# Kernel tuning notes

Hardware: AMD Instinct MI355X
Metric: run time of the kernel (lower is better)

The kernel has to match this reference:

```python
import jax, jax.numpy as jnp
import numpy as np

N_USERS = 100000
M_ITEMS = 50000
N = N_USERS + M_ITEMS
D = 64
NNZ = 4800000
N_LAYERS = 3


def spmm(idx, val, x):
    # sparse COO (idx[0]=rows, idx[1]=cols) @ dense x : gather-scale-scatter
    rows, cols = idx[0], idx[1]
    return jax.ops.segment_sum(val[:, None] * x[cols], rows, num_segments=N)


def propagate(idx, val, emb0):
    # LightGCN propagation: mean over layer-0..n_layers embeddings
    embs = [emb0]
    e = emb0
    for _ in range(N_LAYERS):
        e = spmm(idx, val, e)
        embs.append(e)
    return jnp.mean(jnp.stack(embs, axis=1), axis=1)  # [N, D]


def setup_inputs() -> dict:
    key = jax.random.key(0)
    ks = jax.random.split(key, 10)
    return {
        "emb_im": 0.1 * jax.random.normal(ks[0], (N, D), jnp.float32),
        "emb_q": 0.1 * jax.random.normal(ks[1], (N, D), jnp.float32),
        "emb_p": 0.1 * jax.random.normal(ks[2], (N, D), jnp.float32),
        "g_im_idx": jax.random.randint(ks[3], (2, NNZ), 0, N, jnp.int32),
        "g_im_val": jax.random.uniform(ks[4], (NNZ,), jnp.float32) / 32.0,
        "g_q_idx": jax.random.randint(ks[5], (2, NNZ), 0, N, jnp.int32),
        "g_q_val": jax.random.uniform(ks[6], (NNZ,), jnp.float32) / 32.0,
        "g_p_idx": jax.random.randint(ks[7], (2, NNZ), 0, N, jnp.int32),
        "g_p_val": jax.random.uniform(ks[8], (NNZ,), jnp.float32) / 32.0,
        "add_weight": jnp.ones((3,), jnp.float32),
    }


def reference(emb_im, emb_q, emb_p, g_im_idx, g_im_val, g_q_idx, g_q_val,
              g_p_idx, g_p_val, add_weight):
    out_im = propagate(g_im_idx, g_im_val, emb_im)
    out_q = propagate(g_q_idx, g_q_val, emb_q)
    out_p = propagate(g_p_idx, g_p_val, emb_p)
    # weighted_add over factors: sum_f w_f * out_f ; users/items split is a
    # row split of this combined [N, D] matrix
    stacked = jnp.stack([out_im, out_q, out_p], axis=0)  # [3, N, D]
    combined = jnp.sum(stacked * add_weight[:, None, None], axis=0)  # [N, D]
    return combined  # rows [:N_USERS] = users, rows [N_USERS:] = items
```

## Files before the change

### kernel.cpp

```cpp
#include <hip/hip_runtime.h>

#define N_TOTAL 150000
#define DIM 64
#define RPB 293
#define NBUCK 512
#define MAGIC 14658592u
#define CAP 10368
#define CHUNK 8192

typedef float v2f __attribute__((ext_vector_type(2)));

__global__ void fill_bcur_kernel(int* __restrict__ bcur) {
    int t = blockIdx.x * 256 + threadIdx.x;
    if (t < NBUCK) bcur[t] = t * CAP;
}

__global__ void bin_kernel(const int* __restrict__ idx, const float* __restrict__ val,
                           int* __restrict__ bcur, unsigned* __restrict__ bcs,
                           unsigned short* __restrict__ brl, int nnz) {
    __shared__ unsigned scs[CHUNK];
    __shared__ unsigned srow[CHUNK];
    __shared__ int lcnt[NBUCK];
    __shared__ int lstart[NBUCK];
    __shared__ int gbase[NBUCK];
    __shared__ int wsum[8];
    int t = threadIdx.x;
    int base = blockIdx.x * CHUNK;
    int nEdges = min(CHUNK, nnz - base);
    lcnt[t] = 0;
    __syncthreads();
    unsigned mycs[16];
    int myrow[16], myb[16];
    #pragma unroll
    for (int i = 0; i < 16; ++i) {
        int e = base + t + i * 512;
        if (e < nnz) {
            int r = idx[e];
            int b = (int)__umulhi((unsigned)r, MAGIC);
            myb[i] = b;
            myrow[i] = r;
            unsigned vbits = (__float_as_uint(val[e]) + 0x20000u) & 0xFFFC0000u;
            mycs[i] = vbits | (unsigned)idx[nnz + e];
            atomicAdd(&lcnt[b], 1);
        } else {
            myb[i] = -1;
        }
    }
    __syncthreads();
    int c = lcnt[t];
    int lane = t & 63, wid = t >> 6;
    int incl = c;
    #pragma unroll
    for (int d = 1; d < 64; d <<= 1) {
        int y = __shfl_up(incl, d, 64);
        if (lane >= d) incl += y;
    }
    if (lane == 63) wsum[wid] = incl;
    __syncthreads();
    if (t == 0) {
        int s0 = 0;
        #pragma unroll
        for (int i = 0; i < 8; ++i) { int tmp = wsum[i]; wsum[i] = s0; s0 += tmp; }
    }
    __syncthreads();
    int excl = incl - c + wsum[wid];
    lstart[t] = excl;
    gbase[t] = c ? atomicAdd(&bcur[t], c) : 0;
    lcnt[t] = 0;
    __syncthreads();
    #pragma unroll
    for (int i = 0; i < 16; ++i) {
        int b = myb[i];
        if (b >= 0) {
            int o = atomicAdd(&lcnt[b], 1);
            int p = lstart[b] + o;
            scs[p] = mycs[i];
            srow[p] = (unsigned)myrow[i];
        }
    }
    __syncthreads();
    for (int p = t; p < nEdges; p += 512) {
        int r = (int)srow[p];
        int b = (int)__umulhi((unsigned)r, MAGIC);
        int dst = gbase[b] + (p - lstart[b]);
        if (dst < (b + 1) * CAP) {
            bcs[dst] = scs[p];
            brl[dst] = (unsigned short)(r - b * RPB);
        }
    }
}


__device__ void scatterc_body(int b, const unsigned* __restrict__ bcs,
                              const unsigned short* __restrict__ brl,
                              int* __restrict__ bcur,
                              int* __restrict__ rlo, int* __restrict__ rhi,
                              unsigned* __restrict__ cs2) {
    __shared__ int hist[RPB];
    __shared__ int ssc[256];
    int t = threadIdx.x;
    int s = b * CAP, e = min(bcur[b], s + CAP);
    for (int i = t; i < RPB; i += 256) hist[i] = 0;
    __syncthreads();
    for (int k = s + t; k < e; k += 256)
        atomicAdd(&hist[brl[k]], 1);
    __syncthreads();
    int i0 = 2 * t;
    int c0 = (i0 < RPB) ? hist[i0] : 0;
    int c1 = (i0 + 1 < RPB) ? hist[i0 + 1] : 0;
    int s2 = c0 + c1;
    ssc[t] = s2;
    __syncthreads();
    for (int off = 1; off < 256; off <<= 1) {
        int x = (t >= off) ? ssc[t - off] : 0;
        __syncthreads();
        ssc[t] += x;
        __syncthreads();
    }
    int excl = ssc[t] - s2;
    __syncthreads();
    int base0 = s + excl, base1 = s + excl + c0;
    if (i0 < RPB) {
        int row = b * RPB + i0;
        if (row < N_TOTAL) { rlo[row] = base0; rhi[row] = base0 + c0; }
        hist[i0] = base0;
    }
    if (i0 + 1 < RPB) {
        int row = b * RPB + i0 + 1;
        if (row < N_TOTAL) { rlo[row] = base1; rhi[row] = base1 + c1; }
        hist[i0 + 1] = base1;
    }
    __syncthreads();
    for (int k = s + t; k < e; k += 256) {
        int rl_ = brl[k];
        int o = atomicAdd(&hist[rl_], 1);
        cs2[o] = bcs[k];
    }
    __syncthreads();
    if (t == 0) bcur[b] = s;
}

__device__ void conv_body(int i, const float* __restrict__ x, unsigned* __restrict__ y,
                          int nwords) {
    if (i >= nwords) return;
    int row = i >> 4, w_ = i & 15;
    const float* xr = x + ((size_t)row << 6) + w_;
    int p = __builtin_amdgcn_cvt_pk_fp8_f32(xr[0] * 64.f, xr[16] * 64.f, 0, false);
    p = __builtin_amdgcn_cvt_pk_fp8_f32(xr[32] * 64.f, xr[48] * 64.f, p, true);
    y[i] = (unsigned)p;
}

__device__ inline float4 dec_sum3(const unsigned* __restrict__ T, int i, int nwords) {
    unsigned a = T[i], b = T[i + nwords], c = T[i + 2 * nwords];
    v2f alo = __builtin_amdgcn_cvt_pk_f32_fp8((int)a, false);
    v2f ahi = __builtin_amdgcn_cvt_pk_f32_fp8((int)a, true);
    v2f blo = __builtin_amdgcn_cvt_pk_f32_fp8((int)b, false);
    v2f bhi = __builtin_amdgcn_cvt_pk_f32_fp8((int)b, true);
    v2f clo = __builtin_amdgcn_cvt_pk_f32_fp8((int)c, false);
    v2f chi = __builtin_amdgcn_cvt_pk_f32_fp8((int)c, true);
    float4 r;
    r.x = alo.x + blo.x + clo.x;
    r.y = alo.y + blo.y + clo.y;
    r.z = ahi.x + bhi.x + chi.x;
    r.w = ahi.y + bhi.y + chi.y;
    return r;
}

__device__ void combine_body(int i, const float* __restrict__ emb,
                             const unsigned* __restrict__ T, float c,
                             float* __restrict__ out, int nwords, bool first) {
    if (i >= nwords) return;
    const float kInv = 1.f / 64.f;
    int r = i >> 4, wd = i & 15;
    size_t base = ((size_t)r << 6) + wd;
    float4 s = dec_sum3(T, i, nwords);
    float v0 = c * (emb[base] + kInv * s.x);
    float v1 = c * (emb[base + 16] + kInv * s.y);
    float v2 = c * (emb[base + 32] + kInv * s.z);
    float v3 = c * (emb[base + 48] + kInv * s.w);
    if (first) {
        out[base] = v0; out[base + 16] = v1; out[base + 32] = v2; out[base + 48] = v3;
    } else {
        out[base] += v0; out[base + 16] += v1; out[base + 32] += v2; out[base + 48] += v3;
    }
}

__global__ void scv_kernel(const unsigned* __restrict__ bcs,
                           const unsigned short* __restrict__ brl,
                           int* __restrict__ bcur, int* __restrict__ rlo,
                           int* __restrict__ rhi, unsigned* __restrict__ cs2,
                           const float* __restrict__ embf, unsigned* __restrict__ emb8,
                           const float* __restrict__ embp, const unsigned* __restrict__ Tp,
                           const float* __restrict__ w, int fprev, float* __restrict__ out,
                           int nwords, int nCvt) {
    int b = blockIdx.x;
    if (b < NBUCK) {
        scatterc_body(b, bcs, brl, bcur, rlo, rhi, cs2);
        return;
    }
    b -= NBUCK;
    if (b < nCvt) {
        conv_body(b * 256 + (int)threadIdx.x, embf, emb8, nwords);
        return;
    }
    b -= nCvt;
    combine_body(b * 256 + (int)threadIdx.x, embp, Tp, w[fprev] * 0.25f, out, nwords,
                 fprev == 0);
}

__global__ void combine_kernel(const float* __restrict__ emb, const unsigned* __restrict__ T,
                               const float* __restrict__ w, int f, float* __restrict__ out,
                               int nwords) {
    combine_body(blockIdx.x * 256 + (int)threadIdx.x, emb, T, w[f] * 0.25f, out, nwords,
                 false);
}

__global__ void combine3_kernel(const float* __restrict__ e0, const float* __restrict__ e1,
                                const float* __restrict__ e2, const unsigned* __restrict__ t0,
                                const unsigned* __restrict__ t1, const unsigned* __restrict__ t2,
                                const float* __restrict__ w, float* __restrict__ out,
                                int nwords) {
    int i = blockIdx.x * blockDim.x + threadIdx.x;
    if (i >= nwords) return;
    const float kInv = 1.f / 64.f;
    float c0 = w[0] * 0.25f, c1 = w[1] * 0.25f, c2 = w[2] * 0.25f;
    int r = i >> 4, wd = i & 15;
    size_t base = ((size_t)r << 6) + wd;
    float4 s0 = dec_sum3(t0, i, nwords);
    float4 s1 = dec_sum3(t1, i, nwords);
    float4 s2 = dec_sum3(t2, i, nwords);
    out[base]      = c0 * (e0[base]      + kInv * s0.x) + c1 * (e1[base]      + kInv * s1.x)
                   + c2 * (e2[base]      + kInv * s2.x);
    out[base + 16] = c0 * (e0[base + 16] + kInv * s0.y) + c1 * (e1[base + 16] + kInv * s1.y)
                   + c2 * (e2[base + 16] + kInv * s2.y);
    out[base + 32] = c0 * (e0[base + 32] + kInv * s0.z) + c1 * (e1[base + 32] + kInv * s1.z)
                   + c2 * (e2[base + 32] + kInv * s2.z);
    out[base + 48] = c0 * (e0[base + 48] + kInv * s0.w) + c1 * (e1[base + 48] + kInv * s1.w)
                   + c2 * (e2[base + 48] + kInv * s2.w);
}

__global__ void spmm_reg_kernel(const int* __restrict__ rlo, const int* __restrict__ rhi,
                                const unsigned* __restrict__ cs, const uint2* __restrict__ x2,
                                uint2* __restrict__ y2, int nrows) {
    int gid = blockIdx.x * blockDim.x + threadIdx.x;
    int row = gid >> 6;
    int lane = gid & 63;
    if (row >= nrows) return;
    int s = rlo[row], e = rhi[row];
    int q = lane >> 3, sub = lane & 7;
    v2f a0 = {0.f, 0.f}, a1 = {0.f, 0.f}, a2 = {0.f, 0.f}, a3 = {0.f, 0.f};
    v2f b0 = {0.f, 0.f}, b1 = {0.f, 0.f}, b2 = {0.f, 0.f}, b3 = {0.f, 0.f};
    int k = s + q;
    for (; k + 8 < e; k += 16) {
        unsigned ed0 = cs[k], ed1 = cs[k + 8];
        uint2 g0 = x2[((size_t)(ed0 & 0x3FFFFu) << 3) + sub];
        uint2 g1 = x2[((size_t)(ed1 & 0x3FFFFu) << 3) + sub];
        float v0 = __uint_as_float(ed0 & 0xFFFC0000u);
        float v1 = __uint_as_float(ed1 & 0xFFFC0000u);
        v2f vv0 = {v0, v0}, vv1 = {v1, v1};
        a0 += vv0 * __builtin_amdgcn_cvt_pk_f32_fp8((int)g0.x, false);
        a1 += vv0 * __builtin_amdgcn_cvt_pk_f32_fp8((int)g0.x, true);
        a2 += vv0 * __builtin_amdgcn_cvt_pk_f32_fp8((int)g0.y, false);
        a3 += vv0 * __builtin_amdgcn_cvt_pk_f32_fp8((int)g0.y, true);
        b0 += vv1 * __builtin_amdgcn_cvt_pk_f32_fp8((int)g1.x, false);
        b1 += vv1 * __builtin_amdgcn_cvt_pk_f32_fp8((int)g1.x, true);
        b2 += vv1 * __builtin_amdgcn_cvt_pk_f32_fp8((int)g1.y, false);
        b3 += vv1 * __builtin_amdgcn_cvt_pk_f32_fp8((int)g1.y, true);
    }
    for (; k < e; k += 8) {
        unsigned ed = cs[k];
        uint2 g = x2[((size_t)(ed & 0x3FFFFu) << 3) + sub];
        float vv = __uint_as_float(ed & 0xFFFC0000u);
        v2f vv2 = {vv, vv};
        a0 += vv2 * __builtin_amdgcn_cvt_pk_f32_fp8((int)g.x, false);
        a1 += vv2 * __builtin_amdgcn_cvt_pk_f32_fp8((int)g.x, true);
        a2 += vv2 * __builtin_amdgcn_cvt_pk_f32_fp8((int)g.y, false);
        a3 += vv2 * __builtin_amdgcn_cvt_pk_f32_fp8((int)g.y, true);
    }
    a0 += b0; a1 += b1; a2 += b2; a3 += b3;
    float r0 = a0.x, r1 = a0.y, r2 = a1.x, r3 = a1.y;
    float r4 = a2.x, r5 = a2.y, r6 = a3.x, r7 = a3.y;
    r0 += __shfl_xor(r0, 8); r0 += __shfl_xor(r0, 16); r0 += __shfl_xor(r0, 32);
    r1 += __shfl_xor(r1, 8); r1 += __shfl_xor(r1, 16); r1 += __shfl_xor(r1, 32);
    r2 += __shfl_xor(r2, 8); r2 += __shfl_xor(r2, 16); r2 += __shfl_xor(r2, 32);
    r3 += __shfl_xor(r3, 8); r3 += __shfl_xor(r3, 16); r3 += __shfl_xor(r3, 32);
    r4 += __shfl_xor(r4, 8); r4 += __shfl_xor(r4, 16); r4 += __shfl_xor(r4, 32);
    r5 += __shfl_xor(r5, 8); r5 += __shfl_xor(r5, 16); r5 += __shfl_xor(r5, 32);
    r6 += __shfl_xor(r6, 8); r6 += __shfl_xor(r6, 16); r6 += __shfl_xor(r6, 32);
    r7 += __shfl_xor(r7, 8); r7 += __shfl_xor(r7, 16); r7 += __shfl_xor(r7, 32);
    if (q == 0) {
        int p0 = __builtin_amdgcn_cvt_pk_fp8_f32(r0, r1, 0, false);
        p0 = __builtin_amdgcn_cvt_pk_fp8_f32(r2, r3, p0, true);
        int p1 = __builtin_amdgcn_cvt_pk_fp8_f32(r4, r5, 0, false);
        p1 = __builtin_amdgcn_cvt_pk_fp8_f32(r6, r7, p1, true);
        uint2 o;
        o.x = (unsigned)p0;
        o.y = (unsigned)p1;
        y2[((size_t)row << 3) + sub] = o;
    }
}

extern "C" void kernel_launch(void* const* d_in, const int* in_sizes, int n_in,
                              void* d_out, int out_size, void* d_ws, size_t ws_size,
                              hipStream_t stream) {
    const float* emb[3]  = {(const float*)d_in[0], (const float*)d_in[1], (const float*)d_in[2]};
    const int*   gidx[3] = {(const int*)d_in[3],   (const int*)d_in[5],   (const int*)d_in[7]};
    const float* gval[3] = {(const float*)d_in[4], (const float*)d_in[6], (const float*)d_in[8]};
    const float* w = (const float*)d_in[9];
    float* out = (float*)d_out;

    const int nnz = in_sizes[4];
    const size_t bufElems = (size_t)N_TOTAL * DIM;
    const int nwords = (int)(bufElems / 4);
    const size_t fp8Bytes = (size_t)nwords * 4;
    const size_t capElems = (size_t)NBUCK * CAP;

    char* base = (char*)d_ws;
    unsigned*       bcs  = (unsigned*)base;
    unsigned short* brl  = (unsigned short*)(base + capElems * 4);
    unsigned*       cs2  = (unsigned*)(base + capElems * 6);
    unsigned*       emb8 = (unsigned*)(base + capElems * 10);
    int*            rlo  = (int*)(base + capElems * 10 + fp8Bytes);
    int*            rhi  = rlo + N_TOTAL;
    int*            bcur = rhi + N_TOTAL;
    char*           tab  = (char*)(bcur + NBUCK + 64);
    const size_t needFused = (size_t)(tab - base) + (size_t)9 * fp8Bytes;
    const bool fused = ws_size >= needFused;

    const int nCvt = (nwords + 255) / 256;
    dim3 binGrid((nnz + CHUNK - 1) / CHUNK);
    dim3 rowGrid((unsigned)(((size_t)N_TOTAL * 64 + 255) / 256));
    dim3 cmbGrid((nwords + 255) / 256);

    fill_bcur_kernel<<<2, 256, 0, stream>>>(bcur);

    for (int f = 0; f < 3; ++f) {
        unsigned* tabF = (unsigned*)(tab + (size_t)(fused ? 3 * f : 0) * fp8Bytes);
        unsigned* A8 = tabF;
        unsigned* B8 = tabF + nwords;
        unsigned* C8 = tabF + 2 * (size_t)nwords;

        bin_kernel<<<binGrid, 512, 0, stream>>>(gidx[f], gval[f], bcur, bcs, brl, nnz);

        int hasCmb = (!fused && f > 0) ? 1 : 0;
        const unsigned* Tprev = (const unsigned*)tab;
        const float* embPrev = (f > 0) ? emb[f - 1] : emb[0];
        dim3 scvGrid(NBUCK + nCvt + (hasCmb ? nCvt : 0));
        scv_kernel<<<scvGrid, 256, 0, stream>>>(bcs, brl, bcur, rlo, rhi, cs2,
                                                emb[f], emb8, embPrev, Tprev,
                                                w, f - 1, out, nwords, nCvt);

        spmm_reg_kernel<<<rowGrid, 256, 0, stream>>>(rlo, rhi, cs2, (const uint2*)emb8,
                                                     (uint2*)A8, N_TOTAL);
        spmm_reg_kernel<<<rowGrid, 256, 0, stream>>>(rlo, rhi, cs2, (const uint2*)A8,
                                                     (uint2*)B8, N_TOTAL);
        spmm_reg_kernel<<<rowGrid, 256, 0, stream>>>(rlo, rhi, cs2, (const uint2*)B8,
                                                     (uint2*)C8, N_TOTAL);
    }

    if (fused) {
        const unsigned* t0 = (const unsigned*)tab;
        const unsigned* t1 = t0 + 3 * (size_t)nwords;
        const unsigned* t2 = t0 + 6 * (size_t)nwords;
        combine3_kernel<<<cmbGrid, 256, 0, stream>>>(emb[0], emb[1], emb[2], t0, t1, t2,
                                                     w, out, nwords);
    } else {
        combine_kernel<<<cmbGrid, 256, 0, stream>>>(emb[2], (const unsigned*)tab, w, 2,
                                                    out, nwords);
    }
}
```

Before: 965.6 us.

## Widen SpMM gathers to 16 bytes and streamline binning and bucket scans

The SpMM kernel now has each lane fetch 16 fp8 values as a uint4, so 4 lanes cover a 64-wide row and 16 edges are processed in parallel per wavefront. The goal is fewer, wider gather instructions and more memory parallelism, at the cost of 16 accumulators per lane and a longer shuffle reduction. The bin kernel handles a larger chunk of 19 edges per thread, stores 16-bit local rows instead of full rows in shared memory, and finds each edge's bucket with a binary search over the bucket starts. The scatter kernel replaces its barrier-heavy shared-memory scan with a wave-shuffle scan.

```diff
diff --git a/kernel.cpp b/kernel.cpp
--- a/kernel.cpp
+++ b/kernel.cpp
@@ -6,7 +6,8 @@
 #define NBUCK 512
 #define MAGIC 14658592u
 #define CAP 10368
-#define CHUNK 8192
+#define CHUNK 9375
+#define EPT 19
 
 typedef float v2f __attribute__((ext_vector_type(2)));
 
@@ -19,9 +20,9 @@
                            int* __restrict__ bcur, unsigned* __restrict__ bcs,
                            unsigned short* __restrict__ brl, int nnz) {
     __shared__ unsigned scs[CHUNK];
-    __shared__ unsigned srow[CHUNK];
+    __shared__ unsigned short srl[CHUNK];
     __shared__ int lcnt[NBUCK];
-    __shared__ int lstart[NBUCK];
+    __shared__ int lstart[NBUCK + 1];
     __shared__ int gbase[NBUCK];
     __shared__ int wsum[8];
     int t = threadIdx.x;
@@ -29,21 +30,20 @@
     int nEdges = min(CHUNK, nnz - base);
     lcnt[t] = 0;
     __syncthreads();
-    unsigned mycs[16];
-    int myrow[16], myb[16];
-    #pragma unroll
-    for (int i = 0; i < 16; ++i) {
-        int e = base + t + i * 512;
-        if (e < nnz) {
+    unsigned mycs[EPT];
+    int myrow[EPT];
+    #pragma unroll
+    for (int i = 0; i < EPT; ++i) {
+        int o = t + i * 512;
+        if (o < nEdges) {
+            int e = base + o;
             int r = idx[e];
-            int b = (int)__umulhi((unsigned)r, MAGIC);
-            myb[i] = b;
             myrow[i] = r;
             unsigned vbits = (__float_as_uint(val[e]) + 0x20000u) & 0xFFFC0000u;
             mycs[i] = vbits | (unsigned)idx[nnz + e];
-            atomicAdd(&lcnt[b], 1);
+            atomicAdd(&lcnt[__umulhi((unsigned)r, MAGIC)], 1);
         } else {
-            myb[i] = -1;
+            myrow[i] = -1;
         }
     }
     __syncthreads();
@@ -65,27 +65,32 @@
     __syncthreads();
     int excl = incl - c + wsum[wid];
     lstart[t] = excl;
+    if (t == 511) lstart[NBUCK] = excl + c;
     gbase[t] = c ? atomicAdd(&bcur[t], c) : 0;
     lcnt[t] = 0;
     __syncthreads();
     #pragma unroll
-    for (int i = 0; i < 16; ++i) {
-        int b = myb[i];
-        if (b >= 0) {
+    for (int i = 0; i < EPT; ++i) {
+        int r = myrow[i];
+        if (r >= 0) {
+            int b = (int)__umulhi((unsigned)r, MAGIC);
             int o = atomicAdd(&lcnt[b], 1);
             int p = lstart[b] + o;
             scs[p] = mycs[i];
-            srow[p] = (unsigned)myrow[i];
+            srl[p] = (unsigned short)(r - b * RPB);
         }
     }
     __syncthreads();
     for (int p = t; p < nEdges; p += 512) {
-        int r = (int)srow[p];
-        int b = (int)__umulhi((unsigned)r, MAGIC);
-        int dst = gbase[b] + (p - lstart[b]);
-        if (dst < (b + 1) * CAP) {
+        int lo = 0, hi = NBUCK;
+        while (hi - lo > 1) {
+            int mid = (lo + hi) >> 1;
+            if (lstart[mid] <= p) lo = mid; else hi = mid;
+        }
+        int dst = gbase[lo] + (p - lstart[lo]);
+        if (dst < (lo + 1) * CAP) {
             bcs[dst] = scs[p];
-            brl[dst] = (unsigned short)(r - b * RPB);
+            brl[dst] = srl[p];
         }
     }
 }
@@ -97,7 +102,7 @@
                               int* __restrict__ rlo, int* __restrict__ rhi,
                               unsigned* __restrict__ cs2) {
     __shared__ int hist[RPB];
-    __shared__ int ssc[256];
+    __shared__ int wsum4[4];
     int t = threadIdx.x;
     int s = b * CAP, e = min(bcur[b], s + CAP);
     for (int i = t; i < RPB; i += 256) hist[i] = 0;
@@ -109,17 +114,24 @@
     int c0 = (i0 < RPB) ? hist[i0] : 0;
     int c1 = (i0 + 1 < RPB) ? hist[i0 + 1] : 0;
     int s2 = c0 + c1;
-    ssc[t] = s2;
-    __syncthreads();
-    for (int off = 1; off < 256; off <<= 1) {
-        int x = (t >= off) ? ssc[t - off] : 0;
-        __syncthreads();
-        ssc[t] += x;
-        __syncthreads();
-    }
-    int excl = ssc[t] - s2;
-    __syncthreads();
+    int lane = t & 63, wid = t >> 6;
+    int incl = s2;
+    #pragma unroll
+    for (int d = 1; d < 64; d <<= 1) {
+        int y = __shfl_up(incl, d, 64);
+        if (lane >= d) incl += y;
+    }
+    if (lane == 63) wsum4[wid] = incl;
+    __syncthreads();
+    if (t == 0) {
+        int a0 = 0;
+        #pragma unroll
+        for (int i = 0; i < 4; ++i) { int tmp = wsum4[i]; wsum4[i] = a0; a0 += tmp; }
+    }
+    __syncthreads();
+    int excl = incl - s2 + wsum4[wid];
     int base0 = s + excl, base1 = s + excl + c0;
+    __syncthreads();
     if (i0 < RPB) {
         int row = b * RPB + i0;
         if (row < N_TOTAL) { rlo[row] = base0; rhi[row] = base0 + c0; }
@@ -240,63 +252,83 @@
 }
 
 __global__ void spmm_reg_kernel(const int* __restrict__ rlo, const int* __restrict__ rhi,
-                                const unsigned* __restrict__ cs, const uint2* __restrict__ x2,
-                                uint2* __restrict__ y2, int nrows) {
+                                const unsigned* __restrict__ cs, const uint4* __restrict__ x4,
+                                uint4* __restrict__ y4, int nrows) {
     int gid = blockIdx.x * blockDim.x + threadIdx.x;
     int row = gid >> 6;
     int lane = gid & 63;
     if (row >= nrows) return;
     int s = rlo[row], e = rhi[row];
-    int q = lane >> 3, sub = lane & 7;
-    v2f a0 = {0.f, 0.f}, a1 = {0.f, 0.f}, a2 = {0.f, 0.f}, a3 = {0.f, 0.f};
-    v2f b0 = {0.f, 0.f}, b1 = {0.f, 0.f}, b2 = {0.f, 0.f}, b3 = {0.f, 0.f};
-    int k = s + q;
-    for (; k + 8 < e; k += 16) {
-        unsigned ed0 = cs[k], ed1 = cs[k + 8];
-        uint2 g0 = x2[((size_t)(ed0 & 0x3FFFFu) << 3) + sub];
-        uint2 g1 = x2[((size_t)(ed1 & 0x3FFFFu) << 3) + sub];
+    int g = lane >> 2, sub = lane & 3;
+    v2f a[8], b[8];
+    #pragma unroll
+    for (int j = 0; j < 8; ++j) { a[j] = (v2f){0.f, 0.f}; b[j] = (v2f){0.f, 0.f}; }
+    int k = s + g;
+    for (; k + 16 < e; k += 32) {
+        unsigned ed0 = cs[k], ed1 = cs[k + 16];
+        uint4 g0 = x4[((size_t)(ed0 & 0x3FFFFu) << 2) + sub];
+        uint4 g1 = x4[((size_t)(ed1 & 0x3FFFFu) << 2) + sub];
         float v0 = __uint_as_float(ed0 & 0xFFFC0000u);
         float v1 = __uint_as_float(ed1 & 0xFFFC0000u);
         v2f vv0 = {v0, v0}, vv1 = {v1, v1};
-        a0 += vv0 * __builtin_amdgcn_cvt_pk_f32_fp8((int)g0.x, false);
-        a1 += vv0 * __builtin_amdgcn_cvt_pk_f32_fp8((int)g0.x, true);
-        a2 += vv0 * __builtin_amdgcn_cvt_pk_f32_fp8((int)g0.y, false);
-        a3 += vv0 * __builtin_amdgcn_cvt_pk_f32_fp8((int)g0.y, true);
-        b0 += vv1 * __builtin_amdgcn_cvt_pk_f32_fp8((int)g1.x, false);
-        b1 += vv1 * __builtin_amdgcn_cvt_pk_f32_fp8((int)g1.x, true);
-        b2 += vv1 * __builtin_amdgcn_cvt_pk_f32_fp8((int)g1.y, false);
-        b3 += vv1 * __builtin_amdgcn_cvt_pk_f32_fp8((int)g1.y, true);
-    }
-    for (; k < e; k += 8) {
+        a[0] += vv0 * __builtin_amdgcn_cvt_pk_f32_fp8((int)g0.x, false);
+        a[1] += vv0 * __builtin_amdgcn_cvt_pk_f32_fp8((int)g0.x, true);
+        a[2] += vv0 * __builtin_amdgcn_cvt_pk_f32_fp8((int)g0.y, false);
+        a[3] += vv0 * __builtin_amdgcn_cvt_pk_f32_fp8((int)g0.y, true);
+        a[4] += vv0 * __builtin_amdgcn_cvt_pk_f32_fp8((int)g0.z, false);
+        a[5] += vv0 * __builtin_amdgcn_cvt_pk_f32_fp8((int)g0.z, true);
+        a[6] += vv0 * __builtin_amdgcn_cvt_pk_f32_fp8((int)g0.w, false);
+        a[7] += vv0 * __builtin_amdgcn_cvt_pk_f32_fp8((int)g0.w, true);
+        b[0] += vv1 * __builtin_amdgcn_cvt_pk_f32_fp8((int)g1.x, false);
+        b[1] += vv1 * __builtin_amdgcn_cvt_pk_f32_fp8((int)g1.x, true);
+        b[2] += vv1 * __builtin_amdgcn_cvt_pk_f32_fp8((int)g1.y, false);
+        b[3] += vv1 * __builtin_amdgcn_cvt_pk_f32_fp8((int)g1.y, true);
+        b[4] += vv1 * __builtin_amdgcn_cvt_pk_f32_fp8((int)g1.z, false);
+        b[5] += vv1 * __builtin_amdgcn_cvt_pk_f32_fp8((int)g1.z, true);
+        b[6] += vv1 * __builtin_amdgcn_cvt_pk_f32_fp8((int)g1.w, false);
+        b[7] += vv1 * __builtin_amdgcn_cvt_pk_f32_fp8((int)g1.w, true);
+    }
+    for (; k < e; k += 16) {
         unsigned ed = cs[k];
-        uint2 g = x2[((size_t)(ed & 0x3FFFFu) << 3) + sub];
+        uint4 gg = x4[((size_t)(ed & 0x3FFFFu) << 2) + sub];
         float vv = __uint_as_float(ed & 0xFFFC0000u);
         v2f vv2 = {vv, vv};
-        a0 += vv2 * __builtin_amdgcn_cvt_pk_f32_fp8((int)g.x, false);
-        a1 += vv2 * __builtin_amdgcn_cvt_pk_f32_fp8((int)g.x, true);
-        a2 += vv2 * __builtin_amdgcn_cvt_pk_f32_fp8((int)g.y, false);
-        a3 += vv2 * __builtin_amdgcn_cvt_pk_f32_fp8((int)g.y, true);
-    }
-    a0 += b0; a1 += b1; a2 += b2; a3 += b3;
-    float r0 = a0.x, r1 = a0.y, r2 = a1.x, r3 = a1.y;
-    float r4 = a2.x, r5 = a2.y, r6 = a3.x, r7 = a3.y;
-    r0 += __shfl_xor(r0, 8); r0 += __shfl_xor(r0, 16); r0 += __shfl_xor(r0, 32);
-    r1 += __shfl_xor(r1, 8); r1 += __shfl_xor(r1, 16); r1 += __shfl_xor(r1, 32);
-    r2 += __shfl_xor(r2, 8); r2 += __shfl_xor(r2, 16); r2 += __shfl_xor(r2, 32);
-    r3 += __shfl_xor(r3, 8); r3 += __shfl_xor(r3, 16); r3 += __shfl_xor(r3, 32);
-    r4 += __shfl_xor(r4, 8); r4 += __shfl_xor(r4, 16); r4 += __shfl_xor(r4, 32);
-    r5 += __shfl_xor(r5, 8); r5 += __shfl_xor(r5, 16); r5 += __shfl_xor(r5, 32);
-    r6 += __shfl_xor(r6, 8); r6 += __shfl_xor(r6, 16); r6 += __shfl_xor(r6, 32);
-    r7 += __shfl_xor(r7, 8); r7 += __shfl_xor(r7, 16); r7 += __shfl_xor(r7, 32);
-    if (q == 0) {
-        int p0 = __builtin_amdgcn_cvt_pk_fp8_f32(r0, r1, 0, false);
-        p0 = __builtin_amdgcn_cvt_pk_fp8_f32(r2, r3, p0, true);
-        int p1 = __builtin_amdgcn_cvt_pk_fp8_f32(r4, r5, 0, false);
-        p1 = __builtin_amdgcn_cvt_pk_fp8_f32(r6, r7, p1, true);
-        uint2 o;
-        o.x = (unsigned)p0;
-        o.y = (unsigned)p1;
-        y2[((size_t)row << 3) + sub] = o;
+        a[0] += vv2 * __builtin_amdgcn_cvt_pk_f32_fp8((int)gg.x, false);
+        a[1] += vv2 * __builtin_amdgcn_cvt_pk_f32_fp8((int)gg.x, true);
+        a[2] += vv2 * __builtin_amdgcn_cvt_pk_f32_fp8((int)gg.y, false);
+        a[3] += vv2 * __builtin_amdgcn_cvt_pk_f32_fp8((int)gg.y, true);
+        a[4] += vv2 * __builtin_amdgcn_cvt_pk_f32_fp8((int)gg.z, false);
+        a[5] += vv2 * __builtin_amdgcn_cvt_pk_f32_fp8((int)gg.z, true);
+        a[6] += vv2 * __builtin_amdgcn_cvt_pk_f32_fp8((int)gg.w, false);
+        a[7] += vv2 * __builtin_amdgcn_cvt_pk_f32_fp8((int)gg.w, true);
+    }
+    float r[16];
+    #pragma unroll
+    for (int j = 0; j < 8; ++j) {
+        v2f m = a[j] + b[j];
+        r[2 * j] = m.x;
+        r[2 * j + 1] = m.y;
+    }
+    #pragma unroll
+    for (int j = 0; j < 16; ++j) {
+        float v = r[j];
+        v += __shfl_xor(v, 4);
+        v += __shfl_xor(v, 8);
+        v += __shfl_xor(v, 16);
+        v += __shfl_xor(v, 32);
+        r[j] = v;
+    }
+    if (g == 0) {
+        uint4 o;
+        int p = __builtin_amdgcn_cvt_pk_fp8_f32(r[0], r[1], 0, false);
+        o.x = (unsigned)__builtin_amdgcn_cvt_pk_fp8_f32(r[2], r[3], p, true);
+        p = __builtin_amdgcn_cvt_pk_fp8_f32(r[4], r[5], 0, false);
+        o.y = (unsigned)__builtin_amdgcn_cvt_pk_fp8_f32(r[6], r[7], p, true);
+        p = __builtin_amdgcn_cvt_pk_fp8_f32(r[8], r[9], 0, false);
+        o.z = (unsigned)__builtin_amdgcn_cvt_pk_fp8_f32(r[10], r[11], p, true);
+        p = __builtin_amdgcn_cvt_pk_fp8_f32(r[12], r[13], 0, false);
+        o.w = (unsigned)__builtin_amdgcn_cvt_pk_fp8_f32(r[14], r[15], p, true);
+        y4[((size_t)row << 2) + sub] = o;
     }
 }
 
@@ -350,12 +382,12 @@
                                                 emb[f], emb8, embPrev, Tprev,
                                                 w, f - 1, out, nwords, nCvt);
 
-        spmm_reg_kernel<<<rowGrid, 256, 0, stream>>>(rlo, rhi, cs2, (const uint2*)emb8,
-                                                     (uint2*)A8, N_TOTAL);
-        spmm_reg_kernel<<<rowGrid, 256, 0, stream>>>(rlo, rhi, cs2, (const uint2*)A8,
-                                                     (uint2*)B8, N_TOTAL);
-        spmm_reg_kernel<<<rowGrid, 256, 0, stream>>>(rlo, rhi, cs2, (const uint2*)B8,
-                                                     (uint2*)C8, N_TOTAL);
+        spmm_reg_kernel<<<rowGrid, 256, 0, stream>>>(rlo, rhi, cs2, (const uint4*)emb8,
+                                                     (uint4*)A8, N_TOTAL);
+        spmm_reg_kernel<<<rowGrid, 256, 0, stream>>>(rlo, rhi, cs2, (const uint4*)A8,
+                                                     (uint4*)B8, N_TOTAL);
+        spmm_reg_kernel<<<rowGrid, 256, 0, stream>>>(rlo, rhi, cs2, (const uint4*)B8,
+                                                     (uint4*)C8, N_TOTAL);
     }
 
     if (fused) {
```

Result: slower. 1.242 ms (+28.6%).
